# Performance work log

Measured on AMD Instinct MI355X. Metric: run time of the kernel, lower is better.

## Reference

```python
import jax, jax.numpy as jnp
import numpy as np

B = 2_000_000


def setup_inputs() -> dict:
    key = jax.random.key(0)
    ks = jax.random.split(key, 10)
    b = jax.random.normal(ks[0], (B, 1), dtype=jnp.float32)
    v = jax.random.normal(ks[1], (B, 3), dtype=jnp.float32)
    w = jax.random.normal(ks[2], (B, 3), dtype=jnp.float32)
    dt = jnp.full((1, 1), 0.01, dtype=jnp.float32)
    # params per PhyGate._init_random / linear_b init
    lin_w = jax.random.normal(ks[3], (1, 1), dtype=jnp.float32) * 1e-4
    lin_b = jnp.full((1,), 10.0, dtype=jnp.float32)
    param1 = jax.random.uniform(ks[4], (1, 1), dtype=jnp.float32) * 1e-4
    param2 = jax.random.uniform(ks[5], (1, 1), dtype=jnp.float32) * 1e-4
    param3 = jax.random.uniform(ks[6], (1, 3), dtype=jnp.float32) * 1e-4
    param4 = jax.random.uniform(ks[7], (1,), dtype=jnp.float32) * 1e-4
    param5 = jax.random.uniform(ks[8], (1,), dtype=jnp.float32) * 1e-4
    param6 = jax.random.uniform(ks[9], (1,), dtype=jnp.float32) * 1e-4
    return {"b": b, "v": v, "w": w, "dt": dt, "lin_w": lin_w, "lin_b": lin_b,
            "param1": param1, "param2": param2, "param3": param3,
            "param4": param4, "param5": param5, "param6": param6}


def _phygate(b, v, w, dt, lin_w, lin_b, param1, param2, param3, param4, param5, param6):
    # gate = sigmoid(Linear(1,1)(b)); gate ~ 1 means 'no bounce'
    gate1 = jax.nn.sigmoid(b @ lin_w.T + lin_b)            # [B,1]
    gate2 = 1.0 - gate1
    r = param6                                              # (1,) ball radius
    vx, vy, vz = v[..., 0:1], v[..., 1:2], v[..., 2:3]
    wx, wy, wz = w[..., 0:1], w[..., 1:2], w[..., 2:3]
    # alpha (friction factor), clipped at 0.4
    al = param4 * (1.0 + param5) * jnp.abs(vz) / jnp.sqrt(
        (vx - wy * r) ** 2 + (vy + wx * r) ** 2 + 1e-6)
    al = jnp.where(al > 0.4, 0.4, al)
    # A,B,C,D are diagonal/sparse 3x3 blocks -> compute componentwise
    # (identical math to diag_embed + bmm, without [B,3,3] intermediates)
    one_m_al = 1.0 - al
    v_bc = jnp.concatenate([one_m_al * vx + al * r * wy,
                            one_m_al * vy - al * r * wx,
                            -param5 * vz], axis=-1)         # [B,3]
    c = 1.5 * al / r
    one_m_15al = 1.0 - 1.5 * al
    w_bc = jnp.concatenate([-c * vy + one_m_15al * wx,
                            c * vx + one_m_15al * wy,
                            wz], axis=-1)                   # [B,3]
    v2 = gate1 * v + gate2 * v_bc
    w2 = gate1 * w + gate2 * w_bc
    # Magnus + drag + bias + gravity
    norm_v = jnp.linalg.norm(v2, axis=-1, keepdims=True)    # [B,1]
    cross_vw = jnp.cross(w2, v2)                            # [B,3]
    gravity = jnp.array([0.0, 0.0, -9.81], dtype=v2.dtype)
    acc = -param1 * norm_v * v2 + param2 * cross_vw + param3 + gravity
    v_new = v2 + acc * dt
    return v_new, w2


def reference(b, v, w, dt, lin_w, lin_b, param1, param2, param3, param4, param5, param6):
    return _phygate(b, v, w, dt, lin_w, lin_b, param1, param2, param3, param4, param5, param6)
```

## Files before the change

### kernel.cpp

```cpp
#include <hip/hip_runtime.h>
#include <math.h>


#define SWZ(s) ((s) ^ (((s) >> 3) & 7))

__device__ __forceinline__ void lds_fence() {
    __builtin_amdgcn_wave_barrier();
    asm volatile("" ::: "memory");
}

__device__ __forceinline__ void phygate_row(
    float dt, float lw, float lb, float p1, float p2,
    float p3x, float p3y, float p3z_g, float p5, float r, float rcp_r,
    float coef,
    float bv, float vx, float vy, float vz, float wx, float wy, float wz,
    float& ovx, float& ovy, float& ovz, float& owx, float& owy, float& owz)
{
    float g1 = __builtin_amdgcn_rcpf(1.0f + expf(-(bv * lw + lb)));
    float g2 = 1.0f - g1;

    float dx = vx - wy * r;
    float dy = vy + wx * r;
    float al = coef * fabsf(vz) * __builtin_amdgcn_rsqf(dx * dx + dy * dy + 1e-6f);
    al = fminf(al, 0.4f);

    float oma  = 1.0f - al;
    float alr  = al * r;
    float vbx  = oma * vx + alr * wy;
    float vby  = oma * vy - alr * wx;
    float vbz  = -p5 * vz;

    float c    = 1.5f * al * rcp_r;
    float om15 = 1.0f - 1.5f * al;
    float wbx  = -c * vy + om15 * wx;
    float wby  =  c * vx + om15 * wy;
    float wbz  = wz;

    float v2x = g1 * vx + g2 * vbx;
    float v2y = g1 * vy + g2 * vby;
    float v2z = g1 * vz + g2 * vbz;
    float w2x = g1 * wx + g2 * wbx;
    float w2y = g1 * wy + g2 * wby;
    float w2z = g1 * wz + g2 * wbz;

    float nv = sqrtf(v2x * v2x + v2y * v2y + v2z * v2z);
    float cx = w2y * v2z - w2z * v2y;
    float cy = w2z * v2x - w2x * v2z;
    float cz = w2x * v2y - w2y * v2x;

    float ax = -p1 * nv * v2x + p2 * cx + p3x;
    float ay = -p1 * nv * v2y + p2 * cy + p3y;
    float az = -p1 * nv * v2z + p2 * cz + p3z_g;

    ovx = v2x + ax * dt;
    ovy = v2y + ay * dt;
    ovz = v2z + az * dt;
    owx = w2x;
    owy = w2y;
    owz = w2z;
}

__global__ __launch_bounds__(256, 4) void phygate_kernel(
    const float* __restrict__ b,
    const float* __restrict__ v,
    const float* __restrict__ w,
    const float* __restrict__ dt_p,
    const float* __restrict__ lin_w_p,
    const float* __restrict__ lin_b_p,
    const float* __restrict__ p1_p,
    const float* __restrict__ p2_p,
    const float* __restrict__ p3_p,
    const float* __restrict__ p4_p,
    const float* __restrict__ p5_p,
    const float* __restrict__ p6_p,
    float* __restrict__ out_v,
    float* __restrict__ out_w,
    int B)
{
    const float dt  = dt_p[0];
    const float lw  = lin_w_p[0];
    const float lb  = lin_b_p[0];
    const float p1  = p1_p[0];
    const float p2  = p2_p[0];
    const float p3x = p3_p[0], p3y = p3_p[1];
    const float p3z_g = p3_p[2] - 9.81f;
    const float p4  = p4_p[0];
    const float p5  = p5_p[0];
    const float r   = p6_p[0];
    const float rcp_r = __builtin_amdgcn_rcpf(r);
    const float coef = p4 * (1.0f + p5);

    __shared__ float4 sv[768];
    __shared__ float4 sw[768];

    const int t    = threadIdx.x;
    const int wv   = t >> 6;
    const int lane = t & 63;
    const long long blockRow0 = 1024LL * blockIdx.x;
    const bool full = (blockRow0 + 1024 <= (long long)B);

    if (full) {
        const float4* b4 = (const float4*)b;
        const float4* v4 = (const float4*)v;
        const float4* w4 = (const float4*)w;
        const int tile4 = 768 * blockIdx.x + 192 * wv;
        float4* svw = &sv[192 * wv];
        float4* sww = &sw[192 * wv];

        float4 bb  = b4[256 * blockIdx.x + 64 * wv + lane];
        float4 lv0 = v4[tile4 + lane];
        float4 lv1 = v4[tile4 + lane + 64];
        float4 lv2 = v4[tile4 + lane + 128];
        float4 lw0 = w4[tile4 + lane];
        float4 lw1 = w4[tile4 + lane + 64];
        float4 lw2 = w4[tile4 + lane + 128];

        svw[SWZ(lane)]       = lv0;
        svw[SWZ(lane + 64)]  = lv1;
        svw[SWZ(lane + 128)] = lv2;
        sww[SWZ(lane)]       = lw0;
        sww[SWZ(lane + 64)]  = lw1;
        sww[SWZ(lane + 128)] = lw2;
        lds_fence();

        float4 a0 = svw[SWZ(3 * lane)];
        float4 a1 = svw[SWZ(3 * lane + 1)];
        float4 a2 = svw[SWZ(3 * lane + 2)];
        float4 c0 = sww[SWZ(3 * lane)];
        float4 c1 = sww[SWZ(3 * lane + 1)];
        float4 c2 = sww[SWZ(3 * lane + 2)];

        float vf[12], wf[12], bf4[4], ovf[12], owf[12];
        bf4[0] = bb.x; bf4[1] = bb.y; bf4[2] = bb.z; bf4[3] = bb.w;
        vf[0] = a0.x; vf[1] = a0.y; vf[2]  = a0.z; vf[3]  = a0.w;
        vf[4] = a1.x; vf[5] = a1.y; vf[6]  = a1.z; vf[7]  = a1.w;
        vf[8] = a2.x; vf[9] = a2.y; vf[10] = a2.z; vf[11] = a2.w;
        wf[0] = c0.x; wf[1] = c0.y; wf[2]  = c0.z; wf[3]  = c0.w;
        wf[4] = c1.x; wf[5] = c1.y; wf[6]  = c1.z; wf[7]  = c1.w;
        wf[8] = c2.x; wf[9] = c2.y; wf[10] = c2.z; wf[11] = c2.w;

        #pragma unroll
        for (int j = 0; j < 4; ++j) {
            phygate_row(dt, lw, lb, p1, p2, p3x, p3y, p3z_g, p5, r, rcp_r,
                        coef, bf4[j],
                        vf[3*j], vf[3*j+1], vf[3*j+2],
                        wf[3*j], wf[3*j+1], wf[3*j+2],
                        ovf[3*j], ovf[3*j+1], ovf[3*j+2],
                        owf[3*j], owf[3*j+1], owf[3*j+2]);
        }

        lds_fence();

        svw[SWZ(3 * lane)]     = make_float4(ovf[0], ovf[1], ovf[2],  ovf[3]);
        svw[SWZ(3 * lane + 1)] = make_float4(ovf[4], ovf[5], ovf[6],  ovf[7]);
        svw[SWZ(3 * lane + 2)] = make_float4(ovf[8], ovf[9], ovf[10], ovf[11]);
        sww[SWZ(3 * lane)]     = make_float4(owf[0], owf[1], owf[2],  owf[3]);
        sww[SWZ(3 * lane + 1)] = make_float4(owf[4], owf[5], owf[6],  owf[7]);
        sww[SWZ(3 * lane + 2)] = make_float4(owf[8], owf[9], owf[10], owf[11]);
        lds_fence();

        float4* ov4 = (float4*)out_v;
        float4* ow4 = (float4*)out_w;
        ov4[tile4 + lane]       = svw[SWZ(lane)];
        ov4[tile4 + lane + 64]  = svw[SWZ(lane + 64)];
        ov4[tile4 + lane + 128] = svw[SWZ(lane + 128)];
        ow4[tile4 + lane]       = sww[SWZ(lane)];
        ow4[tile4 + lane + 64]  = sww[SWZ(lane + 64)];
        ow4[tile4 + lane + 128] = sww[SWZ(lane + 128)];
    } else {
        for (int j = 0; j < 4; ++j) {
            long long row = blockRow0 + 4LL * t + j;
            if (row < (long long)B) {
                float vx = v[3 * row], vy = v[3 * row + 1], vz = v[3 * row + 2];
                float wx = w[3 * row], wy = w[3 * row + 1], wz = w[3 * row + 2];
                float ovx, ovy, ovz, owx, owy, owz;
                phygate_row(dt, lw, lb, p1, p2, p3x, p3y, p3z_g, p5, r, rcp_r,
                            coef, b[row], vx, vy, vz, wx, wy, wz,
                            ovx, ovy, ovz, owx, owy, owz);
                out_v[3 * row]     = ovx;
                out_v[3 * row + 1] = ovy;
                out_v[3 * row + 2] = ovz;
                out_w[3 * row]     = owx;
                out_w[3 * row + 1] = owy;
                out_w[3 * row + 2] = owz;
            }
        }
    }
}

extern "C" void kernel_launch(void* const* d_in, const int* in_sizes, int n_in,
                              void* d_out, int out_size, void* d_ws, size_t ws_size,
                              hipStream_t stream) {
    const float* b     = (const float*)d_in[0];
    const float* v     = (const float*)d_in[1];
    const float* w     = (const float*)d_in[2];
    const float* dt    = (const float*)d_in[3];
    const float* lin_w = (const float*)d_in[4];
    const float* lin_b = (const float*)d_in[5];
    const float* p1    = (const float*)d_in[6];
    const float* p2    = (const float*)d_in[7];
    const float* p3    = (const float*)d_in[8];
    const float* p4    = (const float*)d_in[9];
    const float* p5    = (const float*)d_in[10];
    const float* p6    = (const float*)d_in[11];

    const int B = in_sizes[0];
    float* out_v = (float*)d_out;
    float* out_w = out_v + (size_t)3 * B;

    const int threads = 256;
    const int rows_per_block = 1024;
    const int blocks = (B + rows_per_block - 1) / rows_per_block;

    phygate_kernel<<<blocks, threads, 0, stream>>>(
        b, v, w, dt, lin_w, lin_b, p1, p2, p3, p4, p5, p6, out_v, out_w, B);
}
```

Measured before the change: 122.1 us.

## Use persistent grid-stride waves with software-prefetched next tile loads

Replaces the one-block-per-1024-rows launch with a fixed grid of 512 blocks. Each wave loops over 256-row tiles and issues the global loads for its next tile before processing the current one, so memory latency overlaps with compute and LDS shuffling. Tail rows are handled by a single wave, and the launch bounds occupancy hint drops to 2. This costs more registers for the double-buffered tile and fewer waves in flight, which could reduce latency hiding on a purely bandwidth-bound kernel.

Measured after the change: 123.4 us. No clear change (+1.1%).

```diff
diff --git a/kernel.cpp b/kernel.cpp
--- a/kernel.cpp
+++ b/kernel.cpp
@@ -60,7 +60,7 @@
     owz = w2z;
 }
 
-__global__ __launch_bounds__(256, 4) void phygate_kernel(
+__global__ __launch_bounds__(256, 2) void phygate_kernel(
     const float* __restrict__ b,
     const float* __restrict__ v,
     const float* __restrict__ w,
@@ -96,24 +96,48 @@
     const int t    = threadIdx.x;
     const int wv   = t >> 6;
     const int lane = t & 63;
-    const long long blockRow0 = 1024LL * blockIdx.x;
-    const bool full = (blockRow0 + 1024 <= (long long)B);
-
-    if (full) {
-        const float4* b4 = (const float4*)b;
-        const float4* v4 = (const float4*)v;
-        const float4* w4 = (const float4*)w;
-        const int tile4 = 768 * blockIdx.x + 192 * wv;
-        float4* svw = &sv[192 * wv];
-        float4* sww = &sw[192 * wv];
-
-        float4 bb  = b4[256 * blockIdx.x + 64 * wv + lane];
-        float4 lv0 = v4[tile4 + lane];
-        float4 lv1 = v4[tile4 + lane + 64];
-        float4 lv2 = v4[tile4 + lane + 128];
-        float4 lw0 = w4[tile4 + lane];
-        float4 lw1 = w4[tile4 + lane + 64];
-        float4 lw2 = w4[tile4 + lane + 128];
+    float4* svw = &sv[192 * wv];
+    float4* sww = &sw[192 * wv];
+
+    const int waveId = blockIdx.x * 4 + wv;
+    const int nWaves = gridDim.x * 4;
+    const int fullTiles = B >> 8;
+
+    const float4* b4 = (const float4*)b;
+    const float4* v4 = (const float4*)v;
+    const float4* w4 = (const float4*)w;
+    float4* ov4 = (float4*)out_v;
+    float4* ow4 = (float4*)out_w;
+
+    int tile = waveId;
+    bool have = (tile < fullTiles);
+
+    float4 bb, lv0, lv1, lv2, lw0, lw1, lw2;
+    if (have) {
+        const int t4 = 192 * tile;
+        bb  = b4[64 * tile + lane];
+        lv0 = v4[t4 + lane];
+        lv1 = v4[t4 + lane + 64];
+        lv2 = v4[t4 + lane + 128];
+        lw0 = w4[t4 + lane];
+        lw1 = w4[t4 + lane + 64];
+        lw2 = w4[t4 + lane + 128];
+    }
+
+    while (have) {
+        const int nextTile = tile + nWaves;
+        const bool haveNext = (nextTile < fullTiles);
+        float4 nbb, nv0, nv1, nv2, nw0, nw1, nw2;
+        if (haveNext) {
+            const int t4 = 192 * nextTile;
+            nbb = b4[64 * nextTile + lane];
+            nv0 = v4[t4 + lane];
+            nv1 = v4[t4 + lane + 64];
+            nv2 = v4[t4 + lane + 128];
+            nw0 = w4[t4 + lane];
+            nw1 = w4[t4 + lane + 64];
+            nw2 = w4[t4 + lane + 128];
+        }
 
         svw[SWZ(lane)]       = lv0;
         svw[SWZ(lane + 64)]  = lv1;
@@ -159,31 +183,39 @@
         sww[SWZ(3 * lane + 2)] = make_float4(owf[8], owf[9], owf[10], owf[11]);
         lds_fence();
 
-        float4* ov4 = (float4*)out_v;
-        float4* ow4 = (float4*)out_w;
-        ov4[tile4 + lane]       = svw[SWZ(lane)];
-        ov4[tile4 + lane + 64]  = svw[SWZ(lane + 64)];
-        ov4[tile4 + lane + 128] = svw[SWZ(lane + 128)];
-        ow4[tile4 + lane]       = sww[SWZ(lane)];
-        ow4[tile4 + lane + 64]  = sww[SWZ(lane + 64)];
-        ow4[tile4 + lane + 128] = sww[SWZ(lane + 128)];
-    } else {
-        for (int j = 0; j < 4; ++j) {
-            long long row = blockRow0 + 4LL * t + j;
-            if (row < (long long)B) {
-                float vx = v[3 * row], vy = v[3 * row + 1], vz = v[3 * row + 2];
-                float wx = w[3 * row], wy = w[3 * row + 1], wz = w[3 * row + 2];
-                float ovx, ovy, ovz, owx, owy, owz;
-                phygate_row(dt, lw, lb, p1, p2, p3x, p3y, p3z_g, p5, r, rcp_r,
-                            coef, b[row], vx, vy, vz, wx, wy, wz,
-                            ovx, ovy, ovz, owx, owy, owz);
-                out_v[3 * row]     = ovx;
-                out_v[3 * row + 1] = ovy;
-                out_v[3 * row + 2] = ovz;
-                out_w[3 * row]     = owx;
-                out_w[3 * row + 1] = owy;
-                out_w[3 * row + 2] = owz;
-            }
+        {
+            const int t4 = 192 * tile;
+            ov4[t4 + lane]       = svw[SWZ(lane)];
+            ov4[t4 + lane + 64]  = svw[SWZ(lane + 64)];
+            ov4[t4 + lane + 128] = svw[SWZ(lane + 128)];
+            ow4[t4 + lane]       = sww[SWZ(lane)];
+            ow4[t4 + lane + 64]  = sww[SWZ(lane + 64)];
+            ow4[t4 + lane + 128] = sww[SWZ(lane + 128)];
+        }
+        lds_fence();
+
+        tile = nextTile;
+        have = haveNext;
+        bb = nbb;
+        lv0 = nv0; lv1 = nv1; lv2 = nv2;
+        lw0 = nw0; lw1 = nw1; lw2 = nw2;
+    }
+
+    const long long tailStart = (long long)fullTiles * 256;
+    if (waveId == 0) {
+        for (long long row = tailStart + lane; row < (long long)B; row += 64) {
+            float vx = v[3 * row], vy = v[3 * row + 1], vz = v[3 * row + 2];
+            float wx = w[3 * row], wy = w[3 * row + 1], wz = w[3 * row + 2];
+            float ovx, ovy, ovz, owx, owy, owz;
+            phygate_row(dt, lw, lb, p1, p2, p3x, p3y, p3z_g, p5, r, rcp_r,
+                        coef, b[row], vx, vy, vz, wx, wy, wz,
+                        ovx, ovy, ovz, owx, owy, owz);
+            out_v[3 * row]     = ovx;
+            out_v[3 * row + 1] = ovy;
+            out_v[3 * row + 2] = ovz;
+            out_w[3 * row]     = owx;
+            out_w[3 * row + 1] = owy;
+            out_w[3 * row + 2] = owz;
         }
     }
 }
@@ -208,10 +240,12 @@
     float* out_v = (float*)d_out;
     float* out_w = out_v + (size_t)3 * B;
 
-    const int threads = 256;
-    const int rows_per_block = 1024;
-    const int blocks = (B + rows_per_block - 1) / rows_per_block;
-
-    phygate_kernel<<<blocks, threads, 0, stream>>>(
+    const int totalTiles = (B >> 8) > 0 ? (B >> 8) : 1;
+    int blocks = 512;
+    const int maxBlocks = (totalTiles + 3) / 4;
+    if (blocks > maxBlocks) blocks = maxBlocks;
+    if (blocks < 1) blocks = 1;
+
+    phygate_kernel<<<blocks, 256, 0, stream>>>(
         b, v, w, dt, lin_w, lin_b, p1, p2, p3, p4, p5, p6, out_v, out_w, B);
 }
```
